# Performance work log

Measured on AMD Instinct MI355X. Metric: run time of the kernel, lower is better.

The kernel has to match this reference:

```python
import jax, jax.numpy as jnp
import numpy as np

B, L, S, H, D = 4, 2048, 2048, 8, 64


def setup_inputs() -> dict:
    key = jax.random.key(0)
    kq, kk, kv = jax.random.split(key, 3)
    queries = jax.random.normal(kq, (B, L, H, D), dtype=jnp.float32)
    keys = jax.random.normal(kk, (B, S, H, D), dtype=jnp.float32)
    values = jax.random.normal(kv, (B, S, H, D), dtype=jnp.float32)
    # causal mask: True = masked (positions j > i), broadcast to [B, L, S]
    causal = jnp.triu(jnp.ones((L, S), dtype=bool), k=1)
    attn_mask = jnp.broadcast_to(causal, (B, L, S))
    return {"queries": queries, "keys": keys, "values": values, "attn_mask": attn_mask}


def reference(queries, keys, values, attn_mask):
    # queries: [B,L,H,D], keys/values: [B,S,H,D], attn_mask: [B,L,S] bool (True=masked)
    D_ = queries.shape[-1]
    scale = 1.0 / jnp.sqrt(jnp.asarray(D_, dtype=queries.dtype))
    scores = jnp.einsum('blhd,bshd->bhls', queries, keys) * scale  # [B,H,L,S]
    scores = jnp.where(attn_mask[:, None, :, :], -jnp.inf, scores)
    attn = jax.nn.softmax(scores, axis=-1)  # dropout p=0.0 (eval) -> identity
    context = jnp.einsum('bhls,bshd->blhd', attn, values)  # [B,L,H,D]
    return (context, attn)
```

## Files before the change

kernel.cpp:

```cpp
#include <hip/hip_runtime.h>
#include <cstdint>
#include <cstddef>

#define BB 4
#define LL 2048
#define SS 2048
#define HH 8
#define DD 64
#define TQ 64
#define TK 64
#define HD (HH*DD)
#define CTX_N (BB*LL*HH*DD)
#define NBH (BB*HH)
#define NJT (SS/TK)
#define WS_NEED ((size_t)2 * NBH * SS * DD * 2)

using f32x4  = __attribute__((ext_vector_type(4))) float;
using bf16x8 = __attribute__((ext_vector_type(8))) short;
using s16x4  = __attribute__((ext_vector_type(4))) short;

__device__ __forceinline__ short f2bf(float f) {
  union { float f; unsigned u; } v; v.f = f;
  unsigned r = v.u + 0x7FFFu + ((v.u >> 16) & 1u);
  return (short)(r >> 16);
}

__launch_bounds__(256, 4)
__global__ void prep(const float* __restrict__ K, const float* __restrict__ V,
                     short* __restrict__ Kbs, short* __restrict__ Vts) {
  __shared__ float Vl[64][68];
  const int tid = threadIdx.x, bid = blockIdx.x;
  const int bh = bid >> 5, jt = bid & 31;
  const int b = bh >> 3, h = bh & 7;
  const int j0 = jt * 64;
  const int row = tid >> 2, q = tid & 3;

  {
    const float* kp = K + ((size_t)(b*SS + j0 + row)*HH + h)*DD + q*16;
    short* kout = Kbs + ((size_t)bh*SS + j0 + row)*DD + q*16;
    #pragma unroll
    for (int c2 = 0; c2 < 2; ++c2) {
      bf16x8 o;
      #pragma unroll
      for (int i = 0; i < 8; ++i) o[i] = f2bf(kp[c2*8 + i]);
      *(bf16x8*)(kout + c2*8) = o;
    }
  }
  {
    const float* vp = V + ((size_t)(b*SS + j0 + row)*HH + h)*DD + q*16;
    #pragma unroll
    for (int i = 0; i < 4; ++i)
      *(float4*)&Vl[row][q*16 + 4*i] = *(const float4*)(vp + 4*i);
  }
  __syncthreads();
  {
    const int d = tid >> 2, jq = tid & 3;
    short* vout = Vts + (((size_t)bh*NJT + jt)*DD + d)*TK;
    #pragma unroll
    for (int c2 = 0; c2 < 2; ++c2) {
      const int c = jq*2 + c2;
      bf16x8 o;
      #pragma unroll
      for (int i = 0; i < 8; ++i) o[i] = f2bf(Vl[c*8 + i][d]);
      *(bf16x8*)(vout + c*8) = o;
    }
  }
}

__launch_bounds__(256, 4)
__global__ void fa_fwd(const float* __restrict__ Qg,
                       const short* __restrict__ Kbs,
                       const short* __restrict__ Vts,
                       float* __restrict__ Out) {
  __shared__ short Kl[TK*DD];
  __shared__ short Vtl[DD*TK];
  __shared__ float pf[4][16][68];

  const int tid  = threadIdx.x;
  const int wv   = tid >> 6;
  const int lane = tid & 63;
  const int g    = lane >> 4;
  const int r16  = lane & 15;

  const int bid = blockIdx.x;
  const int u   = bid >> 5;
  const int bh  = bid & 31;
  const int u1  = u >> 3, u0 = u & 7;
  const int qrank = (u1 == 0) ? u0 : (u1 == 1) ? (31 - u0) : (u1 == 2) ? (15 - u0) : (16 + u0);
  const int b = bh >> 3, h = bh & 7;
  const int q0  = (31 - qrank) * TQ;
  const int nkt = 32 - qrank;

  const size_t attn_base = (size_t)CTX_N + (size_t)bh * (size_t)LL * (size_t)SS;

  {
    const int jz = q0 + TQ;
    const int n4 = (SS - jz) >> 2;
    if (n4 > 0) {
      f32x4 z = {0.f, 0.f, 0.f, 0.f};
      for (int row = 0; row < TQ; ++row) {
        float* rp = Out + attn_base + (size_t)(q0 + row) * SS + jz;
        for (int c = tid; c < n4; c += 256)
          __builtin_nontemporal_store(z, (f32x4*)(rp + 4*c));
      }
    }
  }

  const float qscale = 0.125f * 1.44269504088896f;
  const float* qptr  = Qg + (size_t)(b*LL + q0 + wv*16 + r16)*HD + h*DD;
  bf16x8 aQ[2];
  #pragma unroll
  for (int s = 0; s < 2; ++s)
    #pragma unroll
    for (int i = 0; i < 8; ++i)
      aQ[s][i] = f2bf(qptr[s*32 + g*8 + i] * qscale);

  auto stage_k = [&](int kt) {
    const short* Kt = Kbs + ((size_t)bh*SS + kt*TK)*DD;
    #pragma unroll
    for (int i = 0; i < 2; ++i) {
      const int ci = wv*128 + i*64 + lane;
      const int row = ci >> 3, c = ci & 7;
      const bf16x8 kv = *(const bf16x8*)(Kt + ci*8);
      *(bf16x8*)((char*)Kl + row*128 + ((c ^ (row & 7)) << 4)) = kv;
    }
  };
  auto stage_v = [&](int kt) {
    const short* Vt = Vts + ((size_t)bh*NJT + kt)*DD*TK;
    #pragma unroll
    for (int i = 0; i < 2; ++i) {
      const int ci = wv*128 + i*64 + lane;
      const int row = ci >> 3, c = ci & 7;
      const bf16x8 vv = *(const bf16x8*)(Vt + ci*8);
      *(bf16x8*)((char*)Vtl + row*128 + ((c ^ (row & 7)) << 4)) = vv;
    }
  };

  auto qk = [&](int j0t, f32x4 (&sacc)[4], bool diag) {
    const int sw = r16 & 7;
    #pragma unroll
    for (int jt = 0; jt < 4; ++jt) {
      const char* base = (const char*)Kl + (jt*16 + r16)*128;
      const bf16x8 bk0 = *(const bf16x8*)(base + (((g    ) ^ sw) << 4));
      const bf16x8 bk1 = *(const bf16x8*)(base + (((4 + g) ^ sw) << 4));
      f32x4 a = {0.f, 0.f, 0.f, 0.f};
      a = __builtin_amdgcn_mfma_f32_16x16x32_bf16(aQ[0], bk0, a, 0, 0, 0);
      a = __builtin_amdgcn_mfma_f32_16x16x32_bf16(aQ[1], bk1, a, 0, 0, 0);
      if (diag) {
        const int jabs = j0t + jt*16 + r16;
        #pragma unroll
        for (int r = 0; r < 4; ++r)
          if (jabs > q0 + wv*16 + g*4 + r) a[r] = -1e30f;
      }
      sacc[jt] = a;
    }
  };

  float lpart[4] = {0.f, 0.f, 0.f, 0.f};
  for (int kt = 0; kt < nkt; ++kt) {
    __syncthreads();
    stage_k(kt);
    __syncthreads();
    f32x4 sacc[4];
    qk(kt * TK, sacc, kt == nkt - 1);
    #pragma unroll
    for (int jt = 0; jt < 4; ++jt)
      #pragma unroll
      for (int r = 0; r < 4; ++r)
        lpart[r] += __builtin_exp2f(sacc[jt][r]);
  }
  float invl[4];
  #pragma unroll
  for (int r = 0; r < 4; ++r) {
    #pragma unroll
    for (int msk = 1; msk < 16; msk <<= 1)
      lpart[r] += __shfl_xor(lpart[r], msk, 64);
    invl[r] = 1.0f / lpart[r];
  }

  f32x4 ctx[4];
  #pragma unroll
  for (int dt = 0; dt < 4; ++dt) ctx[dt] = (f32x4){0.f, 0.f, 0.f, 0.f};

  for (int kt = 0; kt < nkt; ++kt) {
    const int j0 = kt * TK;
    __syncthreads();
    stage_k(kt);
    stage_v(kt);
    __syncthreads();

    f32x4 sacc[4];
    qk(j0, sacc, kt == nkt - 1);

    #pragma unroll
    for (int jt = 0; jt < 4; ++jt)
      #pragma unroll
      for (int r = 0; r < 4; ++r)
        pf[wv][g*4 + r][jt*16 + r16] = __builtin_exp2f(sacc[jt][r]) * invl[r];

    #pragma unroll
    for (int rg = 0; rg < 4; ++rg) {
      const int row = rg*4 + g;
      const f32x4 p4 = *(const f32x4*)&pf[wv][row][r16*4];
      __builtin_nontemporal_store(p4,
        (f32x4*)(Out + attn_base + (size_t)(q0 + wv*16 + row)*SS + j0 + r16*4));
    }

    const int sw = r16 & 7;
    #pragma unroll
    for (int ks = 0; ks < 2; ++ks) {
      const f32x4 pa0 = *(const f32x4*)&pf[wv][r16][ks*32 + g*8];
      const f32x4 pa1 = *(const f32x4*)&pf[wv][r16][ks*32 + g*8 + 4];
      bf16x8 pa;
      #pragma unroll
      for (int i = 0; i < 4; ++i) { pa[i] = f2bf(pa0[i]); pa[4+i] = f2bf(pa1[i]); }
      #pragma unroll
      for (int dt = 0; dt < 4; ++dt) {
        const char* vbase = (const char*)Vtl + (dt*16 + r16)*128;
        const bf16x8 vb = *(const bf16x8*)(vbase + (((ks*4 + g) ^ sw) << 4));
        ctx[dt] = __builtin_amdgcn_mfma_f32_16x16x32_bf16(pa, vb, ctx[dt], 0, 0, 0);
      }
    }
  }

  #pragma unroll
  for (int dt = 0; dt < 4; ++dt)
    #pragma unroll
    for (int r = 0; r < 4; ++r)
      pf[wv][g*4 + r][dt*16 + r16] = ctx[dt][r];
  #pragma unroll
  for (int rg = 0; rg < 4; ++rg) {
    const int row = rg*4 + g;
    const f32x4 c4 = *(const f32x4*)&pf[wv][row][r16*4];
    __builtin_nontemporal_store(c4,
      (f32x4*)(Out + (size_t)(b*LL + q0 + wv*16 + row)*HD + h*DD + r16*4));
  }
}

struct SU {
  union {
    float vs[TK][68];
    float pf[4][16][68];
  };
};

__launch_bounds__(256, 4)
__global__ void fa_fwd_lds(const float* __restrict__ Qg,
                           const float* __restrict__ Kg,
                           const float* __restrict__ Vg,
                           float* __restrict__ Out) {
  __shared__ short Kl[TK][72];
  __shared__ short Vt[DD][72];
  __shared__ SU U;

  const int tid  = threadIdx.x;
  const int wv   = tid >> 6;
  const int lane = tid & 63;
  const int g    = lane >> 4;
  const int r16  = lane & 15;

  const int bid   = blockIdx.x;
  const int qrank = bid >> 5;
  const int bh    = bid & 31;
  const int b     = bh >> 3;
  const int h     = bh & 7;
  const int q0    = (31 - qrank) * TQ;
  const int nkt   = (q0 / TK) + 1;

  const float* Kbh = Kg + (size_t)b*SS*HD + h*DD;
  const float* Vbh = Vg + (size_t)b*SS*HD + h*DD;
  const size_t attn_base = (size_t)CTX_N + (size_t)(b*HH + h) * (size_t)LL * (size_t)SS;

  {
    const int jz = q0 + TQ;
    const int n4 = (SS - jz) >> 2;
    if (n4 > 0) {
      f32x4 z = {0.f, 0.f, 0.f, 0.f};
      for (int row = 0; row < TQ; ++row) {
        float* rp = Out + attn_base + (size_t)(q0 + row) * SS + jz;
        for (int c = tid; c < n4; c += 256)
          __builtin_nontemporal_store(z, (f32x4*)(rp + 4*c));
      }
    }
  }

  const float qscale = 0.125f * 1.44269504088896f;
  const float* qptr  = Qg + (size_t)(b*LL + q0 + wv*16 + r16)*HD + h*DD;
  bf16x8 aQ[2];
  #pragma unroll
  for (int s = 0; s < 2; ++s)
    #pragma unroll
    for (int i = 0; i < 8; ++i)
      aQ[s][i] = f2bf(qptr[s*32 + g*8 + i] * qscale);

  auto stage_k = [&](int j0) {
    #pragma unroll
    for (int c = 0; c < 4; ++c) {
      const int chunk = tid + c*256;
      const int row = chunk >> 4, c4 = chunk & 15;
      const float4 kv = *(const float4*)(Kbh + (size_t)(j0 + row)*HD + c4*4);
      s16x4 s4; s4[0] = f2bf(kv.x); s4[1] = f2bf(kv.y); s4[2] = f2bf(kv.z); s4[3] = f2bf(kv.w);
      *(s16x4*)&Kl[row][c4*4] = s4;
    }
  };

  auto compute_s = [&](int j0, f32x4 (&sacc)[4], bool diag) {
    #pragma unroll
    for (int jt = 0; jt < 4; ++jt) {
      bf16x8 bk0 = *(const bf16x8*)&Kl[jt*16 + r16][g*8];
      bf16x8 bk1 = *(const bf16x8*)&Kl[jt*16 + r16][32 + g*8];
      f32x4 a = {0.f, 0.f, 0.f, 0.f};
      a = __builtin_amdgcn_mfma_f32_16x16x32_bf16(aQ[0], bk0, a, 0, 0, 0);
      a = __builtin_amdgcn_mfma_f32_16x16x32_bf16(aQ[1], bk1, a, 0, 0, 0);
      if (diag) {
        const int jabs = j0 + jt*16 + r16;
        #pragma unroll
        for (int r = 0; r < 4; ++r) {
          if (jabs > q0 + wv*16 + g*4 + r) a[r] = -1e30f;
        }
      }
      sacc[jt] = a;
    }
  };

  float lpart[4] = {0.f, 0.f, 0.f, 0.f};
  for (int kt = 0; kt < nkt; ++kt) {
    __syncthreads();
    stage_k(kt * TK);
    __syncthreads();
    f32x4 sacc[4];
    compute_s(kt * TK, sacc, kt == nkt - 1);
    #pragma unroll
    for (int r = 0; r < 4; ++r)
      #pragma unroll
      for (int jt = 0; jt < 4; ++jt)
        lpart[r] += __builtin_exp2f(sacc[jt][r]);
  }
  float invl[4];
  #pragma unroll
  for (int r = 0; r < 4; ++r) {
    #pragma unroll
    for (int msk = 1; msk < 16; msk <<= 1)
      lpart[r] += __shfl_xor(lpart[r], msk, 64);
    invl[r] = 1.0f / lpart[r];
  }

  f32x4 ctx[4];
  #pragma unroll
  for (int dt = 0; dt < 4; ++dt) ctx[dt] = (f32x4){0.f, 0.f, 0.f, 0.f};

  for (int kt = 0; kt < nkt; ++kt) {
    const int j0 = kt * TK;
    __syncthreads();
    stage_k(j0);
    #pragma unroll
    for (int c = 0; c < 4; ++c) {
      const int chunk = tid + c*256;
      const int row = chunk >> 4, c4 = chunk & 15;
      const float4 vv = *(const float4*)(Vbh + (size_t)(j0 + row)*HD + c4*4);
      *(float4*)&U.vs[row][c4*4] = vv;
    }
    __syncthreads();
    #pragma unroll
    for (int c = 0; c < 4; ++c) {
      const float4 vv = *(const float4*)&U.vs[lane][wv*16 + c*4];
      Vt[wv*16 + c*4 + 0][lane] = f2bf(vv.x);
      Vt[wv*16 + c*4 + 1][lane] = f2bf(vv.y);
      Vt[wv*16 + c*4 + 2][lane] = f2bf(vv.z);
      Vt[wv*16 + c*4 + 3][lane] = f2bf(vv.w);
    }
    __syncthreads();

    f32x4 sacc[4];
    compute_s(j0, sacc, kt == nkt - 1);

    #pragma unroll
    for (int jt = 0; jt < 4; ++jt)
      #pragma unroll
      for (int r = 0; r < 4; ++r)
        U.pf[wv][g*4 + r][jt*16 + r16] = __builtin_exp2f(sacc[jt][r]) * invl[r];

    #pragma unroll
    for (int rg = 0; rg < 4; ++rg) {
      const int row = rg*4 + g;
      const f32x4 p4 = *(const f32x4*)&U.pf[wv][row][r16*4];
      __builtin_nontemporal_store(p4,
        (f32x4*)(Out + attn_base + (size_t)(q0 + wv*16 + row)*SS + j0 + r16*4));
    }

    #pragma unroll
    for (int ks = 0; ks < 2; ++ks) {
      const f32x4 pa0 = *(const f32x4*)&U.pf[wv][r16][ks*32 + g*8];
      const f32x4 pa1 = *(const f32x4*)&U.pf[wv][r16][ks*32 + g*8 + 4];
      bf16x8 pa;
      #pragma unroll
      for (int i = 0; i < 4; ++i) { pa[i] = f2bf(pa0[i]); pa[4+i] = f2bf(pa1[i]); }
      #pragma unroll
      for (int dt = 0; dt < 4; ++dt) {
        bf16x8 vb = *(const bf16x8*)&Vt[dt*16 + r16][ks*32 + g*8];
        ctx[dt] = __builtin_amdgcn_mfma_f32_16x16x32_bf16(pa, vb, ctx[dt], 0, 0, 0);
      }
    }
  }

  #pragma unroll
  for (int dt = 0; dt < 4; ++dt)
    #pragma unroll
    for (int r = 0; r < 4; ++r)
      U.pf[wv][g*4 + r][dt*16 + r16] = ctx[dt][r];
  #pragma unroll
  for (int rg = 0; rg < 4; ++rg) {
    const int row = rg*4 + g;
    const f32x4 c4 = *(const f32x4*)&U.pf[wv][row][r16*4];
    __builtin_nontemporal_store(c4,
      (f32x4*)(Out + (size_t)(b*LL + q0 + wv*16 + row)*HD + h*DD + r16*4));
  }
}

extern "C" void kernel_launch(void* const* d_in, const int* in_sizes, int n_in,
                              void* d_out, int out_size, void* d_ws, size_t ws_size,
                              hipStream_t stream) {
  const float* Q = (const float*)d_in[0];
  const float* K = (const float*)d_in[1];
  const float* V = (const float*)d_in[2];
  float* Out = (float*)d_out;
  if (ws_size >= WS_NEED) {
    short* Kbs = (short*)d_ws;
    short* Vts = Kbs + (size_t)NBH*SS*DD;
    prep<<<dim3(NBH*NJT), dim3(256), 0, stream>>>(K, V, Kbs, Vts);
    fa_fwd<<<dim3(BB*HH*(LL/TQ)), dim3(256), 0, stream>>>(Q, Kbs, Vts, Out);
  } else {
    fa_fwd_lds<<<dim3(BB*HH*(LL/TQ)), dim3(256), 0, stream>>>(Q, K, V, Out);
  }
}
```

Measured before the change: 146.0 us.

## Use 128-wide key tiles and load transposed V directly from global

Key tiles widen from 64 to 128 columns, which halves the number of barrier-separated iterations. V is now pre-transposed into a [bh][D][S] layout, and its MFMA operands are loaded straight from global into registers instead of being staged through LDS. The block-to-query-tile mapping changes from the interleaved balancing order to plain descending work order. The attention-row stores now cover 128 contiguous floats per half-wave. This raises register and LDS use (launch bounds lowered to 3), and for even query tiles the last key tile computes up to 64 extra masked columns.

```diff
diff --git a/kernel.cpp b/kernel.cpp
--- a/kernel.cpp
+++ b/kernel.cpp
@@ -8,11 +8,9 @@
 #define HH 8
 #define DD 64
 #define TQ 64
-#define TK 64
 #define HD (HH*DD)
 #define CTX_N (BB*LL*HH*DD)
 #define NBH (BB*HH)
-#define NJT (SS/TK)
 #define WS_NEED ((size_t)2 * NBH * SS * DD * 2)
 
 using f32x4  = __attribute__((ext_vector_type(4))) float;
@@ -30,14 +28,14 @@
                      short* __restrict__ Kbs, short* __restrict__ Vts) {
   __shared__ float Vl[64][68];
   const int tid = threadIdx.x, bid = blockIdx.x;
-  const int bh = bid >> 5, jt = bid & 31;
+  const int bh = bid >> 5, sblk = bid & 31;
   const int b = bh >> 3, h = bh & 7;
-  const int j0 = jt * 64;
+  const int s0 = sblk * 64;
   const int row = tid >> 2, q = tid & 3;
 
   {
-    const float* kp = K + ((size_t)(b*SS + j0 + row)*HH + h)*DD + q*16;
-    short* kout = Kbs + ((size_t)bh*SS + j0 + row)*DD + q*16;
+    const float* kp = K + ((size_t)(b*SS + s0 + row)*HH + h)*DD + q*16;
+    short* kout = Kbs + ((size_t)bh*SS + s0 + row)*DD + q*16;
     #pragma unroll
     for (int c2 = 0; c2 < 2; ++c2) {
       bf16x8 o;
@@ -47,34 +45,32 @@
     }
   }
   {
-    const float* vp = V + ((size_t)(b*SS + j0 + row)*HH + h)*DD + q*16;
+    const float* vp = V + ((size_t)(b*SS + s0 + row)*HH + h)*DD + q*16;
     #pragma unroll
     for (int i = 0; i < 4; ++i)
       *(float4*)&Vl[row][q*16 + 4*i] = *(const float4*)(vp + 4*i);
   }
   __syncthreads();
   {
-    const int d = tid >> 2, jq = tid & 3;
-    short* vout = Vts + (((size_t)bh*NJT + jt)*DD + d)*TK;
-    #pragma unroll
-    for (int c2 = 0; c2 < 2; ++c2) {
-      const int c = jq*2 + c2;
-      bf16x8 o;
-      #pragma unroll
-      for (int i = 0; i < 8; ++i) o[i] = f2bf(Vl[c*8 + i][d]);
-      *(bf16x8*)(vout + c*8) = o;
+    const int d = tid >> 2, sc = (tid & 3) * 16;
+    short* vout = Vts + ((size_t)bh*DD + d)*SS + s0 + sc;
+    #pragma unroll
+    for (int i = 0; i < 4; ++i) {
+      s16x4 o;
+      #pragma unroll
+      for (int k = 0; k < 4; ++k) o[k] = f2bf(Vl[sc + 4*i + k][d]);
+      *(s16x4*)(vout + 4*i) = o;
     }
   }
 }
 
-__launch_bounds__(256, 4)
+__launch_bounds__(256, 3)
 __global__ void fa_fwd(const float* __restrict__ Qg,
                        const short* __restrict__ Kbs,
                        const short* __restrict__ Vts,
                        float* __restrict__ Out) {
-  __shared__ short Kl[TK*DD];
-  __shared__ short Vtl[DD*TK];
-  __shared__ float pf[4][16][68];
+  __shared__ short Kl[128*64];
+  __shared__ float pf[4][16][132];
 
   const int tid  = threadIdx.x;
   const int wv   = tid >> 6;
@@ -85,16 +81,15 @@
   const int bid = blockIdx.x;
   const int u   = bid >> 5;
   const int bh  = bid & 31;
-  const int u1  = u >> 3, u0 = u & 7;
-  const int qrank = (u1 == 0) ? u0 : (u1 == 1) ? (31 - u0) : (u1 == 2) ? (15 - u0) : (16 + u0);
+  const int m   = 31 - u;
   const int b = bh >> 3, h = bh & 7;
-  const int q0  = (31 - qrank) * TQ;
-  const int nkt = 32 - qrank;
+  const int q0  = m * TQ;
+  const int nkt = (m >> 1) + 1;
 
   const size_t attn_base = (size_t)CTX_N + (size_t)bh * (size_t)LL * (size_t)SS;
 
   {
-    const int jz = q0 + TQ;
+    const int jz = nkt * 128;
     const int n4 = (SS - jz) >> 2;
     if (n4 > 0) {
       f32x4 z = {0.f, 0.f, 0.f, 0.f};
@@ -115,31 +110,24 @@
     for (int i = 0; i < 8; ++i)
       aQ[s][i] = f2bf(qptr[s*32 + g*8 + i] * qscale);
 
-  auto stage_k = [&](int kt) {
-    const short* Kt = Kbs + ((size_t)bh*SS + kt*TK)*DD;
-    #pragma unroll
-    for (int i = 0; i < 2; ++i) {
-      const int ci = wv*128 + i*64 + lane;
+  const short* Kbh = Kbs + (size_t)bh * SS * DD;
+  const short* Vbh = Vts + (size_t)bh * DD * SS;
+
+  auto stage_k = [&](int t) {
+    const short* Kt = Kbh + (size_t)t * 128 * DD;
+    #pragma unroll
+    for (int i = 0; i < 4; ++i) {
+      const int ci = i*256 + tid;
       const int row = ci >> 3, c = ci & 7;
       const bf16x8 kv = *(const bf16x8*)(Kt + ci*8);
-      *(bf16x8*)((char*)Kl + row*128 + ((c ^ (row & 7)) << 4)) = kv;
+      *(bf16x8*)(Kl + (row*8 + (c ^ (row & 7)))*8) = kv;
     }
   };
-  auto stage_v = [&](int kt) {
-    const short* Vt = Vts + ((size_t)bh*NJT + kt)*DD*TK;
-    #pragma unroll
-    for (int i = 0; i < 2; ++i) {
-      const int ci = wv*128 + i*64 + lane;
-      const int row = ci >> 3, c = ci & 7;
-      const bf16x8 vv = *(const bf16x8*)(Vt + ci*8);
-      *(bf16x8*)((char*)Vtl + row*128 + ((c ^ (row & 7)) << 4)) = vv;
-    }
-  };
-
-  auto qk = [&](int j0t, f32x4 (&sacc)[4], bool diag) {
+
+  auto qk = [&](int j0t, f32x4 (&sacc)[8], bool diag) {
     const int sw = r16 & 7;
     #pragma unroll
-    for (int jt = 0; jt < 4; ++jt) {
+    for (int jt = 0; jt < 8; ++jt) {
       const char* base = (const char*)Kl + (jt*16 + r16)*128;
       const bf16x8 bk0 = *(const bf16x8*)(base + (((g    ) ^ sw) << 4));
       const bf16x8 bk1 = *(const bf16x8*)(base + (((4 + g) ^ sw) << 4));
@@ -157,14 +145,14 @@
   };
 
   float lpart[4] = {0.f, 0.f, 0.f, 0.f};
-  for (int kt = 0; kt < nkt; ++kt) {
-    __syncthreads();
-    stage_k(kt);
-    __syncthreads();
-    f32x4 sacc[4];
-    qk(kt * TK, sacc, kt == nkt - 1);
-    #pragma unroll
-    for (int jt = 0; jt < 4; ++jt)
+  for (int t = 0; t < nkt; ++t) {
+    __syncthreads();
+    stage_k(t);
+    __syncthreads();
+    f32x4 sacc[8];
+    qk(t * 128, sacc, t == nkt - 1);
+    #pragma unroll
+    for (int jt = 0; jt < 8; ++jt)
       #pragma unroll
       for (int r = 0; r < 4; ++r)
         lpart[r] += __builtin_exp2f(sacc[jt][r]);
@@ -182,44 +170,49 @@
   #pragma unroll
   for (int dt = 0; dt < 4; ++dt) ctx[dt] = (f32x4){0.f, 0.f, 0.f, 0.f};
 
-  for (int kt = 0; kt < nkt; ++kt) {
-    const int j0 = kt * TK;
-    __syncthreads();
-    stage_k(kt);
-    stage_v(kt);
-    __syncthreads();
-
-    f32x4 sacc[4];
-    qk(j0, sacc, kt == nkt - 1);
-
-    #pragma unroll
-    for (int jt = 0; jt < 4; ++jt)
+  const int srow2 = lane >> 5;
+  const int c32   = (lane & 31) * 4;
+
+  for (int t = 0; t < nkt; ++t) {
+    const int j0 = t * 128;
+    __syncthreads();
+    stage_k(t);
+    __syncthreads();
+
+    bf16x8 vb[4][4];
+    #pragma unroll
+    for (int ks = 0; ks < 4; ++ks)
+      #pragma unroll
+      for (int dt = 0; dt < 4; ++dt)
+        vb[ks][dt] = *(const bf16x8*)(Vbh + (size_t)(dt*16 + r16)*SS + j0 + ks*32 + g*8);
+
+    f32x4 sacc[8];
+    qk(j0, sacc, t == nkt - 1);
+
+    #pragma unroll
+    for (int jt = 0; jt < 8; ++jt)
       #pragma unroll
       for (int r = 0; r < 4; ++r)
         pf[wv][g*4 + r][jt*16 + r16] = __builtin_exp2f(sacc[jt][r]) * invl[r];
 
     #pragma unroll
-    for (int rg = 0; rg < 4; ++rg) {
-      const int row = rg*4 + g;
-      const f32x4 p4 = *(const f32x4*)&pf[wv][row][r16*4];
+    for (int rg = 0; rg < 8; ++rg) {
+      const int row = rg*2 + srow2;
+      const f32x4 p4 = *(const f32x4*)&pf[wv][row][c32];
       __builtin_nontemporal_store(p4,
-        (f32x4*)(Out + attn_base + (size_t)(q0 + wv*16 + row)*SS + j0 + r16*4));
-    }
-
-    const int sw = r16 & 7;
-    #pragma unroll
-    for (int ks = 0; ks < 2; ++ks) {
+        (f32x4*)(Out + attn_base + (size_t)(q0 + wv*16 + row)*SS + j0 + c32));
+    }
+
+    #pragma unroll
+    for (int ks = 0; ks < 4; ++ks) {
       const f32x4 pa0 = *(const f32x4*)&pf[wv][r16][ks*32 + g*8];
       const f32x4 pa1 = *(const f32x4*)&pf[wv][r16][ks*32 + g*8 + 4];
       bf16x8 pa;
       #pragma unroll
       for (int i = 0; i < 4; ++i) { pa[i] = f2bf(pa0[i]); pa[4+i] = f2bf(pa1[i]); }
       #pragma unroll
-      for (int dt = 0; dt < 4; ++dt) {
-        const char* vbase = (const char*)Vtl + (dt*16 + r16)*128;
-        const bf16x8 vb = *(const bf16x8*)(vbase + (((ks*4 + g) ^ sw) << 4));
-        ctx[dt] = __builtin_amdgcn_mfma_f32_16x16x32_bf16(pa, vb, ctx[dt], 0, 0, 0);
-      }
+      for (int dt = 0; dt < 4; ++dt)
+        ctx[dt] = __builtin_amdgcn_mfma_f32_16x16x32_bf16(pa, vb[ks][dt], ctx[dt], 0, 0, 0);
     }
   }
 
@@ -239,7 +232,7 @@
 
 struct SU {
   union {
-    float vs[TK][68];
+    float vs[64][68];
     float pf[4][16][68];
   };
 };
@@ -249,7 +242,7 @@
                            const float* __restrict__ Kg,
                            const float* __restrict__ Vg,
                            float* __restrict__ Out) {
-  __shared__ short Kl[TK][72];
+  __shared__ short Kl[64][72];
   __shared__ short Vt[DD][72];
   __shared__ SU U;
 
@@ -265,7 +258,7 @@
   const int b     = bh >> 3;
   const int h     = bh & 7;
   const int q0    = (31 - qrank) * TQ;
-  const int nkt   = (q0 / TK) + 1;
+  const int nkt   = (q0 / 64) + 1;
 
   const float* Kbh = Kg + (size_t)b*SS*HD + h*DD;
   const float* Vbh = Vg + (size_t)b*SS*HD + h*DD;
@@ -326,10 +319,10 @@
   float lpart[4] = {0.f, 0.f, 0.f, 0.f};
   for (int kt = 0; kt < nkt; ++kt) {
     __syncthreads();
-    stage_k(kt * TK);
+    stage_k(kt * 64);
     __syncthreads();
     f32x4 sacc[4];
-    compute_s(kt * TK, sacc, kt == nkt - 1);
+    compute_s(kt * 64, sacc, kt == nkt - 1);
     #pragma unroll
     for (int r = 0; r < 4; ++r)
       #pragma unroll
@@ -350,7 +343,7 @@
   for (int dt = 0; dt < 4; ++dt) ctx[dt] = (f32x4){0.f, 0.f, 0.f, 0.f};
 
   for (int kt = 0; kt < nkt; ++kt) {
-    const int j0 = kt * TK;
+    const int j0 = kt * 64;
     __syncthreads();
     stage_k(j0);
     #pragma unroll
@@ -427,7 +420,7 @@
   if (ws_size >= WS_NEED) {
     short* Kbs = (short*)d_ws;
     short* Vts = Kbs + (size_t)NBH*SS*DD;
-    prep<<<dim3(NBH*NJT), dim3(256), 0, stream>>>(K, V, Kbs, Vts);
+    prep<<<dim3(NBH*(SS/64)), dim3(256), 0, stream>>>(K, V, Kbs, Vts);
     fa_fwd<<<dim3(BB*HH*(LL/TQ)), dim3(256), 0, stream>>>(Q, Kbs, Vts, Out);
   } else {
     fa_fwd_lds<<<dim3(BB*HH*(LL/TQ)), dim3(256), 0, stream>>>(Q, K, V, Out);
```

Measured after the change: 177.5 us. +21.6%, slower.
